# Kernel optimization log

Hardware: AMD Instinct MI355X
Metric: run time of the kernel (lower is better)

The kernel has to match this reference:

```python
import jax, jax.numpy as jnp
import numpy as np

C_M, C_Z, H, C_HID = 256, 128, 8, 32
N_SEQ, N_RES = 64, 384
INF = 1e9
EPS = 1e-5


def layernorm(x, w, b):
    mu = jnp.mean(x, axis=-1, keepdims=True)
    var = jnp.mean(jnp.square(x - mu), axis=-1, keepdims=True)
    return (x - mu) * jax.lax.rsqrt(var + EPS) * w + b


def setup_inputs() -> dict:
    key = jax.random.key(0)
    ks = jax.random.split(key, 6)
    m = jax.random.normal(ks[0], (N_SEQ, N_RES, C_M), dtype=jnp.float32)
    z = jax.random.normal(ks[1], (N_RES, N_RES, C_Z), dtype=jnp.float32)
    mask = jnp.ones((N_SEQ, N_RES), dtype=jnp.float32)
    return {
        "m": m,
        "z": z,
        "mask": mask,
        "ln_m_w": jnp.ones((C_M,), jnp.float32),
        "ln_m_b": jnp.zeros((C_M,), jnp.float32),
        "ln_z_w": jnp.ones((C_Z,), jnp.float32),
        "ln_z_b": jnp.zeros((C_Z,), jnp.float32),
        "W_z": jax.random.normal(ks[2], (C_Z, H), jnp.float32) * 0.05,
        "W_v": jax.random.normal(ks[3], (C_M, H * C_HID), jnp.float32) * 0.05,
        "W_g": jax.random.normal(ks[4], (C_M, H * C_HID), jnp.float32) * 0.05,
        "W_o": jax.random.normal(ks[5], (H * C_HID, C_M), jnp.float32) * 0.05,
    }


def reference(m, z, mask, ln_m_w, ln_m_b, ln_z_w, ln_z_b, W_z, W_v, W_g, W_o):
    S, N = m.shape[0], m.shape[1]
    # mask: max over MSA rows, keepdim -> [1, N]; bias -> [1,1,1,N]
    mask_max = jnp.max(mask, axis=-2, keepdims=True)
    mask_bias = (INF * (mask_max - 1.0))[:, None, None, :]  # [1,1,1,N]
    # pair bias: LN(z) @ W_z -> [N,N,H] -> [H,N,N]
    zb = layernorm(z, ln_z_w, ln_z_b) @ W_z  # [N,N,H]
    zb = jnp.transpose(zb, (2, 0, 1))  # [H,N,N]
    # LN on m
    m_ln = layernorm(m, ln_m_w, ln_m_b)  # [S,N,C_m]
    # values: [S,N,H*c] -> [S,H,N,c]
    v = (m_ln @ W_v).reshape(S, N, H, C_HID).transpose(0, 2, 1, 3)
    # attention weights from summed biases (no QK): [1,H,N,N] after broadcast
    a = jax.nn.softmax(mask_bias + zb[None], axis=-1)  # [1,H,N,N]
    # o = a @ v  -> [S,H,N,c]
    o = jnp.einsum('hqk,shkc->shqc', a[0], v)
    o = o.transpose(0, 2, 1, 3)  # [S,N,H,c]
    # sigmoid gate
    g = jax.nn.sigmoid(m_ln @ W_g).reshape(S, N, H, C_HID)
    o = (o * g).reshape(S, N, H * C_HID)
    return o @ W_o  # [S,N,C_m]
```

## Files before the change

### kernel.cpp

```cpp
#include <hip/hip_runtime.h>
#include <math.h>

#define S 64
#define NRES 384
#define CM 256
#define CZ 128
#define NH 8
#define CH 32
#define HC 256
#define NROW 147456

typedef unsigned short u16;
typedef __attribute__((ext_vector_type(8))) short bf16x8;
typedef __attribute__((ext_vector_type(4))) float f32x4;
typedef __attribute__((ext_vector_type(8))) unsigned short ushort8;
typedef __attribute__((ext_vector_type(4))) unsigned short ushort4_t;

#define OFF_BIAS 0
#define OFF_WWT  8192
#define OFF_C1   16384
#define OFF_C2   16448
#define OFF_WT   200704
#define OFF_WOT  462848
#define OFF_A    593920
#define OFF_VT   2953216
#define OFF_G    15536128
#define OFF_O    28119040
#define OFF_MLN  40701952
#define OFF_ZB   OFF_O

__device__ __forceinline__ u16 f2bf(float f) {
    union { float f; unsigned int u; } v; v.f = f;
    unsigned int u = v.u;
    u += 0x7fff + ((u >> 16) & 1);
    return (u16)(u >> 16);
}
__device__ __forceinline__ float bf2f(u16 b) {
    union { float f; unsigned int u; } v; v.u = ((unsigned int)b) << 16;
    return v.f;
}
__device__ __forceinline__ void gload16(const u16* g, u16* l) {
    __builtin_amdgcn_global_load_lds(
        (const __attribute__((address_space(1))) void*)g,
        (__attribute__((address_space(3))) void*)l, 16, 0, 0);
}

__global__ __launch_bounds__(256) void k_misc(
        const float* __restrict__ mask, const float* __restrict__ Wz,
        const float* __restrict__ lzw, const float* __restrict__ lzb,
        const float* __restrict__ Wv, const float* __restrict__ Wg,
        const float* __restrict__ Wo, const float* __restrict__ m,
        const float* __restrict__ lmw, const float* __restrict__ lmb,
        float* __restrict__ bias, u16* __restrict__ WWT,
        float* __restrict__ C1, float* __restrict__ C2,
        u16* __restrict__ Wt, u16* __restrict__ Wot, u16* __restrict__ mln) {
    __shared__ float sP[2][2][8];
    const int bid = blockIdx.x, tid = threadIdx.x;
    if (bid < 2) {
        const int k = bid * 256 + tid;
        if (k < NRES) {
            float mx = -1e30f;
            for (int s = 0; s < S; ++s) mx = fmaxf(mx, mask[s * NRES + k]);
            bias[k] = 1e9f * (mx - 1.0f);
        }
    } else if (bid == 2) {
        const int wave = tid >> 6, lane = tid & 63;
        if (tid < 128) {
            const int c = tid;
            const float4 wz0 = *(const float4*)&Wz[c * 8];
            const float4 wz1 = *(const float4*)&Wz[c * 8 + 4];
            const float lw = lzw[c], lbv = lzb[c];
            float wzv[8] = {wz0.x, wz0.y, wz0.z, wz0.w, wz1.x, wz1.y, wz1.z, wz1.w};
            float ww[8], wb[8];
            #pragma unroll
            for (int h = 0; h < 8; ++h) {
                ww[h] = lw * wzv[h];
                wb[h] = lbv * wzv[h];
                WWT[h * 128 + c] = f2bf(ww[h]);
                WWT[(8 + h) * 128 + c] = 0;
            }
            #pragma unroll
            for (int h = 0; h < 8; ++h) {
                #pragma unroll
                for (int off = 1; off < 64; off <<= 1) {
                    ww[h] += __shfl_xor(ww[h], off);
                    wb[h] += __shfl_xor(wb[h], off);
                }
            }
            if (lane == 0) {
                #pragma unroll
                for (int h = 0; h < 8; ++h) {
                    sP[wave][0][h] = ww[h];
                    sP[wave][1][h] = wb[h];
                }
            }
        }
        __syncthreads();
        if (tid < 8) {
            C1[tid] = sP[0][0][tid] + sP[1][0][tid];
            C2[tid] = sP[0][1][tid] + sP[1][1][tid];
        }
    } else if (bid < 515) {
        const int i = (bid - 3) * 256 + tid;
        const int n = i >> 8, k = i & 255;
        const float v = (n < HC) ? Wv[(size_t)k * HC + n] : Wg[(size_t)k * HC + (n - HC)];
        Wt[i] = f2bf(v);
    } else if (bid < 771) {
        const int i = (bid - 515) * 256 + tid;
        const int n = i >> 8, k = i & 255;
        Wot[i] = f2bf(Wo[(size_t)k * CM + n]);
    } else {
        const int row = (bid - 771) * 4 + (tid >> 6);
        const int lane = tid & 63;
        const float4 x = *(const float4*)&m[(size_t)row * CM + lane * 4];
        float sm = x.x + x.y + x.z + x.w;
        float sq = x.x*x.x + x.y*x.y + x.z*x.z + x.w*x.w;
        #pragma unroll
        for (int off = 32; off >= 1; off >>= 1) {
            sm += __shfl_xor(sm, off);
            sq += __shfl_xor(sq, off);
        }
        const float mu = sm * (1.0f / CM);
        const float var = sq * (1.0f / CM) - mu * mu;
        const float rs = rsqrtf(var + 1e-5f);
        const float4 w4 = *(const float4*)&lmw[lane * 4];
        const float4 b4 = *(const float4*)&lmb[lane * 4];
        u16 t4[4];
        t4[0] = f2bf((x.x - mu) * rs * w4.x + b4.x);
        t4[1] = f2bf((x.y - mu) * rs * w4.y + b4.y);
        t4[2] = f2bf((x.z - mu) * rs * w4.z + b4.z);
        t4[3] = f2bf((x.w - mu) * rs * w4.w + b4.w);
        *(ushort4_t*)&mln[(size_t)row * CM + lane * 4] = *(ushort4_t*)t4;
    }
}

__global__ __launch_bounds__(256) void k_zb(
        const float* __restrict__ z, const u16* __restrict__ WWT,
        const float* __restrict__ C1, const float* __restrict__ C2,
        float* __restrict__ zb) {
    __shared__ u16 sZ[4][2048];
    __shared__ float sSt[4][2][16];
    const int tid = threadIdx.x, wave = tid >> 6, lane = tid & 63;
    const int rl = lane & 15, kg = lane >> 4;
    u16* myZ = &sZ[wave][0];
    bf16x8 bfr[4];
    #pragma unroll
    for (int t = 0; t < 4; ++t)
        bfr[t] = *(const bf16x8*)&WWT[rl * 128 + t * 32 + kg * 8];
    const float c1 = (rl < 8) ? C1[rl] : 0.f;
    const float c2 = (rl < 8) ? C2[rl] : 0.f;

    #pragma unroll 1
    for (int it = 0; it < 4; ++it) {
        const int row0 = (blockIdx.x * 4 + it) * 64 + wave * 16;
        const float4* zbase = (const float4*)(z + (size_t)row0 * CZ);
        float smj[4], sqj[4];
        #pragma unroll
        for (int j = 0; j < 4; ++j) {
            const int ci = lane + 64 * j;
            const int rloc = ci >> 4, ch = ci & 15;
            const float4 x0 = zbase[ci * 2];
            const float4 x1 = zbase[ci * 2 + 1];
            float xs[8] = {x0.x, x0.y, x0.z, x0.w, x1.x, x1.y, x1.z, x1.w};
            float sm = 0.f, sq = 0.f;
            u16 t8[8];
            #pragma unroll
            for (int e = 0; e < 8; ++e) {
                sm += xs[e]; sq += xs[e] * xs[e];
                t8[e] = f2bf(xs[e]);
            }
            smj[j] = sm; sqj[j] = sq;
            *(ushort8*)&myZ[rloc * 128 + (ch ^ (rloc & 7)) * 8] = *(ushort8*)t8;
        }
        #pragma unroll
        for (int j = 0; j < 4; ++j) {
            #pragma unroll
            for (int off = 1; off < 16; off <<= 1) {
                smj[j] += __shfl_xor(smj[j], off);
                sqj[j] += __shfl_xor(sqj[j], off);
            }
        }
        if ((lane & 15) == 0) {
            #pragma unroll
            for (int j = 0; j < 4; ++j) {
                const int r = (lane >> 4) + 4 * j;
                const float mu = smj[j] * (1.0f / CZ);
                const float var = sqj[j] * (1.0f / CZ) - mu * mu;
                sSt[wave][0][r] = mu;
                sSt[wave][1][r] = rsqrtf(var + 1e-5f);
            }
        }
        bf16x8 af[4];
        #pragma unroll
        for (int t = 0; t < 4; ++t)
            af[t] = *(const bf16x8*)&myZ[rl * 128 + ((t * 4 + kg) ^ (rl & 7)) * 8];
        f32x4 acc = {};
        #pragma unroll
        for (int t = 0; t < 4; ++t)
            acc = __builtin_amdgcn_mfma_f32_16x16x32_bf16(af[t], bfr[t], acc, 0, 0, 0);
        f32x4 pv;
        #pragma unroll
        for (int r = 0; r < 4; ++r) {
            const int rr = kg * 4 + r;
            pv[r] = sSt[wave][1][rr] * (acc[r] - sSt[wave][0][rr] * c1) + c2;
        }
        if (rl < 8)
            *(f32x4*)&zb[(size_t)rl * NROW + row0 + kg * 4] = pv;
    }
}

__global__ __launch_bounds__(256) void k_stage2(
        const u16* __restrict__ mln, const u16* __restrict__ Wt,
        const float* __restrict__ zb, const float* __restrict__ bias,
        u16* __restrict__ vt, u16* __restrict__ g_, u16* __restrict__ a_out) {
    __shared__ u16 As[128][32];
    __shared__ u16 Bs[128][32];
    const int bid = blockIdx.x, tid = threadIdx.x;
    if (bid >= 768) {
        const int w = (bid - 768) * 4 + (tid >> 6);
        const int lane = tid & 63;
        const int h = w & 7, q = w >> 3;
        const float* zbh = zb + (size_t)h * NROW + (size_t)q * NRES;
        float v[6];
        float mx = -1e30f;
        #pragma unroll
        for (int t = 0; t < 6; ++t) {
            const int k = lane + 64 * t;
            v[t] = zbh[k] + bias[k];
            mx = fmaxf(mx, v[t]);
        }
        #pragma unroll
        for (int off = 32; off >= 1; off >>= 1) mx = fmaxf(mx, __shfl_xor(mx, off));
        float sum = 0.f;
        #pragma unroll
        for (int t = 0; t < 6; ++t) { v[t] = expf(v[t] - mx); sum += v[t]; }
        #pragma unroll
        for (int off = 32; off >= 1; off >>= 1) sum += __shfl_xor(sum, off);
        const float inv = 1.0f / sum;
        #pragma unroll
        for (int t = 0; t < 6; ++t)
            a_out[((size_t)h * NRES + q) * NRES + lane + 64 * t] = f2bf(v[t] * inv);
        return;
    }
    const int xcd = bid & 7, idx = bid >> 3;
    const int nt = idx & 3, mt = xcd * 24 + (idx >> 2);
    const int m0 = mt * 128, n0 = nt * 128;
    const int wave = tid >> 6, lane = tid & 63;
    const int wm = (wave >> 1) * 64, wn = (wave & 1) * 64;
    const int rl = lane & 15, kg = lane >> 4;
    const int lr = lane >> 2, lk = (lane & 3) * 8;
    const int wr = wave * 32;
    const u16* ag  = mln + (size_t)(m0 + wr + lr) * CM + lk;
    const u16* ag2 = ag + 16 * CM;
    const u16* bg  = Wt + (size_t)(n0 + wr + lr) * CM + lk;
    const u16* bg2 = bg + 16 * CM;
    u16* al  = &As[wr][0];
    u16* al2 = &As[wr + 16][0];
    u16* bl  = &Bs[wr][0];
    u16* bl2 = &Bs[wr + 16][0];
    const bool vhalf = (n0 < HC);
    f32x4 acc[4][4] = {};
    for (int kt = 0; kt < CM; kt += 32) {
        if (kt) __syncthreads();
        gload16(ag + kt, al);  gload16(ag2 + kt, al2);
        gload16(bg + kt, bl);  gload16(bg2 + kt, bl2);
        __syncthreads();
        bf16x8 af[4], bfr[4];
        #pragma unroll
        for (int i = 0; i < 4; ++i) af[i]  = *(const bf16x8*)&As[wm + i*16 + rl][kg*8];
        #pragma unroll
        for (int j = 0; j < 4; ++j) bfr[j] = *(const bf16x8*)&Bs[wn + j*16 + rl][kg*8];
        if (vhalf) {
            #pragma unroll
            for (int j = 0; j < 4; ++j)
                #pragma unroll
                for (int i = 0; i < 4; ++i)
                    acc[j][i] = __builtin_amdgcn_mfma_f32_16x16x32_bf16(bfr[j], af[i], acc[j][i], 0, 0, 0);
        } else {
            #pragma unroll
            for (int i = 0; i < 4; ++i)
                #pragma unroll
                for (int j = 0; j < 4; ++j)
                    acc[i][j] = __builtin_amdgcn_mfma_f32_16x16x32_bf16(af[i], bfr[j], acc[i][j], 0, 0, 0);
        }
    }
    if (vhalf) {
        #pragma unroll
        for (int j = 0; j < 4; ++j)
            #pragma unroll
            for (int r = 0; r < 4; ++r) {
                const int vcol = n0 + wn + j*16 + kg*4 + r;
                const int h = vcol >> 5, c = vcol & 31;
                #pragma unroll
                for (int i = 0; i < 4; ++i) {
                    const int mrowb = m0 + wm + i*16;
                    const int s = mrowb / NRES;
                    const int nn = mrowb - s * NRES + rl;
                    vt[(((size_t)h * S + s) * CH + c) * NRES + nn] = f2bf(acc[j][i][r]);
                }
            }
    } else {
        #pragma unroll
        for (int i = 0; i < 4; ++i)
            #pragma unroll
            for (int r = 0; r < 4; ++r) {
                const int row = m0 + wm + i*16 + kg*4 + r;
                #pragma unroll
                for (int j = 0; j < 4; ++j) {
                    const int gc = n0 + wn + j*16 + rl - HC;
                    g_[(size_t)row * HC + gc] = f2bf(1.0f / (1.0f + expf(-acc[i][j][r])));
                }
            }
    }
}

__global__ __launch_bounds__(256) void k_attn2(const u16* __restrict__ a_,
        const u16* __restrict__ vt, u16* __restrict__ o_) {
    __shared__ u16 As[128][32];
    __shared__ u16 Bs[128][32];
    const int tid = threadIdx.x;
    const int h = blockIdx.x & 7, rem = blockIdx.x >> 3;
    const int mt = rem >> 4, nt = rem & 15;
    const int q0 = mt * 128, sc0 = nt * 128;
    const int wave = tid >> 6, lane = tid & 63;
    const int wm = (wave >> 1) * 64, wn = (wave & 1) * 64;
    const int rl = lane & 15, kg = lane >> 4;
    const int lr = lane >> 2, lk = (lane & 3) * 8;
    const int wr = wave * 32;
    const u16* ag  = a_ + (size_t)h * NRES * NRES + (size_t)(q0 + wr + lr) * NRES + lk;
    const u16* ag2 = ag + 16 * NRES;
    const u16* bg  = vt + (size_t)h * S * CH * NRES + (size_t)(sc0 + wr + lr) * NRES + lk;
    const u16* bg2 = bg + 16 * NRES;
    u16* al  = &As[wr][0];
    u16* al2 = &As[wr + 16][0];
    u16* bl  = &Bs[wr][0];
    u16* bl2 = &Bs[wr + 16][0];
    f32x4 acc[4][4] = {};
    for (int kt = 0; kt < NRES; kt += 32) {
        if (kt) __syncthreads();
        gload16(ag + kt, al);  gload16(ag2 + kt, al2);
        gload16(bg + kt, bl);  gload16(bg2 + kt, bl2);
        __syncthreads();
        bf16x8 af[4], bfr[4];
        #pragma unroll
        for (int i = 0; i < 4; ++i) af[i]  = *(const bf16x8*)&As[wm + i*16 + rl][kg*8];
        #pragma unroll
        for (int j = 0; j < 4; ++j) bfr[j] = *(const bf16x8*)&Bs[wn + j*16 + rl][kg*8];
        #pragma unroll
        for (int i = 0; i < 4; ++i)
            #pragma unroll
            for (int j = 0; j < 4; ++j)
                acc[i][j] = __builtin_amdgcn_mfma_f32_16x16x32_bf16(af[i], bfr[j], acc[i][j], 0, 0, 0);
    }
    #pragma unroll
    for (int i = 0; i < 4; ++i)
        #pragma unroll
        for (int r = 0; r < 4; ++r) {
            const int q = q0 + wm + i*16 + kg*4 + r;
            #pragma unroll
            for (int j = 0; j < 4; ++j) {
                const int sc = sc0 + wn + j*16 + rl;
                const int s = sc >> 5, c = sc & 31;
                o_[(((size_t)s * NRES + q) * NH + h) * CH + c] = f2bf(acc[i][j][r]);
            }
        }
}

__global__ __launch_bounds__(256) void k_gemm_out(const u16* __restrict__ o_,
        const u16* __restrict__ g_, const u16* __restrict__ Wot,
        float* __restrict__ out) {
    __shared__ u16 As[128][40];
    __shared__ u16 Bs[128][32];
    const int tid = threadIdx.x;
    const int xcd = blockIdx.x & 7, idx = blockIdx.x >> 3;
    const int nt = idx & 1, mt = xcd * 24 + (idx >> 1);
    const int m0 = mt * 128, n0 = nt * 128;
    const int wave = tid >> 6, lane = tid & 63;
    const int wm = (wave >> 1) * 64, wn = (wave & 1) * 64;
    const int rl = lane & 15, kg = lane >> 4;
    const int lr = lane >> 2, lk = (lane & 3) * 8;
    const int wr = wave * 32;
    const int sr = tid >> 1, sh = (tid & 1) * 16;
    const u16* orow = o_ + (size_t)(m0 + sr) * HC;
    const u16* grow = g_ + (size_t)(m0 + sr) * HC;
    const u16* bg  = Wot + (size_t)(n0 + wr + lr) * HC + lk;
    const u16* bg2 = bg + 16 * HC;
    u16* bl  = &Bs[wr][0];
    u16* bl2 = &Bs[wr + 16][0];
    f32x4 acc[4][4] = {};
    for (int kt = 0; kt < HC; kt += 32) {
        if (kt) __syncthreads();
        gload16(bg + kt, bl);  gload16(bg2 + kt, bl2);
        {
            u16 tmp[16];
            const ushort8 ov0 = *(const ushort8*)&orow[kt + sh];
            const ushort8 ov1 = *(const ushort8*)&orow[kt + sh + 8];
            const ushort8 gv0 = *(const ushort8*)&grow[kt + sh];
            const ushort8 gv1 = *(const ushort8*)&grow[kt + sh + 8];
            #pragma unroll
            for (int p = 0; p < 8; ++p) {
                tmp[p]     = f2bf(bf2f(ov0[p]) * bf2f(gv0[p]));
                tmp[p + 8] = f2bf(bf2f(ov1[p]) * bf2f(gv1[p]));
            }
            *(ushort8*)&As[sr][sh]     = *(ushort8*)&tmp[0];
            *(ushort8*)&As[sr][sh + 8] = *(ushort8*)&tmp[8];
        }
        __syncthreads();
        bf16x8 af[4], bfr[4];
        #pragma unroll
        for (int i = 0; i < 4; ++i) af[i]  = *(const bf16x8*)&As[wm + i*16 + rl][kg*8];
        #pragma unroll
        for (int j = 0; j < 4; ++j) bfr[j] = *(const bf16x8*)&Bs[wn + j*16 + rl][kg*8];
        #pragma unroll
        for (int i = 0; i < 4; ++i)
            #pragma unroll
            for (int j = 0; j < 4; ++j)
                acc[i][j] = __builtin_amdgcn_mfma_f32_16x16x32_bf16(af[i], bfr[j], acc[i][j], 0, 0, 0);
    }
    #pragma unroll
    for (int i = 0; i < 4; ++i)
        #pragma unroll
        for (int r = 0; r < 4; ++r) {
            const int row = m0 + wm + i*16 + kg*4 + r;
            #pragma unroll
            for (int j = 0; j < 4; ++j)
                out[(size_t)row * CM + n0 + wn + j*16 + rl] = acc[i][j][r];
        }
}

extern "C" void kernel_launch(void* const* d_in, const int* in_sizes, int n_in,
                              void* d_out, int out_size, void* d_ws, size_t ws_size,
                              hipStream_t stream) {
    const float* m      = (const float*)d_in[0];
    const float* z      = (const float*)d_in[1];
    const float* mask   = (const float*)d_in[2];
    const float* ln_m_w = (const float*)d_in[3];
    const float* ln_m_b = (const float*)d_in[4];
    const float* ln_z_w = (const float*)d_in[5];
    const float* ln_z_b = (const float*)d_in[6];
    const float* Wz     = (const float*)d_in[7];
    const float* Wv     = (const float*)d_in[8];
    const float* Wg     = (const float*)d_in[9];
    const float* Wo     = (const float*)d_in[10];
    float* out = (float*)d_out;
    char* ws = (char*)d_ws;

    float* bias = (float*)(ws + OFF_BIAS);
    u16* WWT    = (u16*)(ws + OFF_WWT);
    float* C1   = (float*)(ws + OFF_C1);
    float* C2   = (float*)(ws + OFF_C2);
    u16* Wt     = (u16*)(ws + OFF_WT);
    u16* Wot    = (u16*)(ws + OFF_WOT);
    u16* a      = (u16*)(ws + OFF_A);
    u16* vtw    = (u16*)(ws + OFF_VT);
    u16* gw     = (u16*)(ws + OFF_G);
    u16* ow     = (u16*)(ws + OFF_O);
    u16* mlnw   = (u16*)(ws + OFF_MLN);
    float* zbw  = (float*)(ws + OFF_ZB);

    k_misc<<<6915, 256, 0, stream>>>(mask, Wz, ln_z_w, ln_z_b, Wv, Wg, Wo, m,
                                     ln_m_w, ln_m_b, bias, WWT, C1, C2, Wt, Wot, mlnw);
    k_zb<<<576, 256, 0, stream>>>(z, WWT, C1, C2, zbw);
    k_stage2<<<1536, 256, 0, stream>>>(mlnw, Wt, zbw, bias, vtw, gw, a);
    k_attn2<<<384, 256, 0, stream>>>(a, vtw, ow);
    k_gemm_out<<<384, 256, 0, stream>>>(ow, gw, Wot, out);
}
```

Measured before the change: 85.45 us.

## Spread z-bias kernel over more blocks with up-front loads, parallelize mask max

The pair-bias kernel drops its 4-iteration loop per block and launches four times as many blocks, each handling one 64-row tile. Each thread issues all eight float4 loads of its tile up front, so more memory traffic is in flight at once. The per-row statistics now reduce across 32 lanes with contiguous float4 loads instead of strided 8-wide chunks. The mask max-reduction is split across 6 blocks and 4 waves, with a shared-memory combine replacing the serial 64-row loop per thread.

New measurement: 76.59 us. 10.4% less time.

```diff
diff --git a/kernel.cpp b/kernel.cpp
--- a/kernel.cpp
+++ b/kernel.cpp
@@ -45,7 +45,7 @@
         (__attribute__((address_space(3))) void*)l, 16, 0, 0);
 }
 
-__global__ __launch_bounds__(256) void k_misc(
+__global__ __launch_bounds__(256) void k_pre(
         const float* __restrict__ mask, const float* __restrict__ Wz,
         const float* __restrict__ lzw, const float* __restrict__ lzb,
         const float* __restrict__ Wv, const float* __restrict__ Wg,
@@ -54,17 +54,26 @@
         float* __restrict__ bias, u16* __restrict__ WWT,
         float* __restrict__ C1, float* __restrict__ C2,
         u16* __restrict__ Wt, u16* __restrict__ Wot, u16* __restrict__ mln) {
-    __shared__ float sP[2][2][8];
+    __shared__ float sRed[4][64];
     const int bid = blockIdx.x, tid = threadIdx.x;
-    if (bid < 2) {
-        const int k = bid * 256 + tid;
-        if (k < NRES) {
-            float mx = -1e30f;
-            for (int s = 0; s < S; ++s) mx = fmaxf(mx, mask[s * NRES + k]);
+    const int wave = tid >> 6, lane = tid & 63;
+    if (bid < 6) {
+        const int k = bid * 64 + lane;
+        float mx = -1e30f;
+        #pragma unroll
+        for (int i = 0; i < 16; ++i) {
+            const int s = wave * 16 + i;
+            mx = fmaxf(mx, mask[(size_t)s * NRES + k]);
+        }
+        sRed[wave][lane] = mx;
+        __syncthreads();
+        if (wave == 0) {
+            mx = fmaxf(fmaxf(sRed[0][lane], sRed[1][lane]),
+                       fmaxf(sRed[2][lane], sRed[3][lane]));
             bias[k] = 1e9f * (mx - 1.0f);
         }
-    } else if (bid == 2) {
-        const int wave = tid >> 6, lane = tid & 63;
+    } else if (bid == 6) {
+        __shared__ float sP[2][2][8];
         if (tid < 128) {
             const int c = tid;
             const float4 wz0 = *(const float4*)&Wz[c * 8];
@@ -100,18 +109,17 @@
             C1[tid] = sP[0][0][tid] + sP[1][0][tid];
             C2[tid] = sP[0][1][tid] + sP[1][1][tid];
         }
-    } else if (bid < 515) {
-        const int i = (bid - 3) * 256 + tid;
+    } else if (bid < 519) {
+        const int i = (bid - 7) * 256 + tid;
         const int n = i >> 8, k = i & 255;
         const float v = (n < HC) ? Wv[(size_t)k * HC + n] : Wg[(size_t)k * HC + (n - HC)];
         Wt[i] = f2bf(v);
-    } else if (bid < 771) {
-        const int i = (bid - 515) * 256 + tid;
+    } else if (bid < 775) {
+        const int i = (bid - 519) * 256 + tid;
         const int n = i >> 8, k = i & 255;
         Wot[i] = f2bf(Wo[(size_t)k * CM + n]);
     } else {
-        const int row = (bid - 771) * 4 + (tid >> 6);
-        const int lane = tid & 63;
+        const int row = (bid - 775) * 4 + wave;
         const float4 x = *(const float4*)&m[(size_t)row * CM + lane * 4];
         float sm = x.x + x.y + x.z + x.w;
         float sq = x.x*x.x + x.y*x.y + x.z*x.z + x.w*x.w;
@@ -143,70 +151,69 @@
     const int tid = threadIdx.x, wave = tid >> 6, lane = tid & 63;
     const int rl = lane & 15, kg = lane >> 4;
     u16* myZ = &sZ[wave][0];
+    const int row0 = blockIdx.x * 64 + wave * 16;
+    const float4* zbase = (const float4*)(z + (size_t)row0 * CZ);
+    float4 xb[8];
+    #pragma unroll
+    for (int j = 0; j < 8; ++j) xb[j] = zbase[lane + 64 * j];
     bf16x8 bfr[4];
     #pragma unroll
     for (int t = 0; t < 4; ++t)
         bfr[t] = *(const bf16x8*)&WWT[rl * 128 + t * 32 + kg * 8];
     const float c1 = (rl < 8) ? C1[rl] : 0.f;
     const float c2 = (rl < 8) ? C2[rl] : 0.f;
-
-    #pragma unroll 1
-    for (int it = 0; it < 4; ++it) {
-        const int row0 = (blockIdx.x * 4 + it) * 64 + wave * 16;
-        const float4* zbase = (const float4*)(z + (size_t)row0 * CZ);
-        float smj[4], sqj[4];
-        #pragma unroll
-        for (int j = 0; j < 4; ++j) {
-            const int ci = lane + 64 * j;
-            const int rloc = ci >> 4, ch = ci & 15;
-            const float4 x0 = zbase[ci * 2];
-            const float4 x1 = zbase[ci * 2 + 1];
-            float xs[8] = {x0.x, x0.y, x0.z, x0.w, x1.x, x1.y, x1.z, x1.w};
-            float sm = 0.f, sq = 0.f;
-            u16 t8[8];
-            #pragma unroll
-            for (int e = 0; e < 8; ++e) {
-                sm += xs[e]; sq += xs[e] * xs[e];
-                t8[e] = f2bf(xs[e]);
-            }
-            smj[j] = sm; sqj[j] = sq;
-            *(ushort8*)&myZ[rloc * 128 + (ch ^ (rloc & 7)) * 8] = *(ushort8*)t8;
-        }
-        #pragma unroll
-        for (int j = 0; j < 4; ++j) {
-            #pragma unroll
-            for (int off = 1; off < 16; off <<= 1) {
-                smj[j] += __shfl_xor(smj[j], off);
-                sqj[j] += __shfl_xor(sqj[j], off);
-            }
-        }
-        if ((lane & 15) == 0) {
-            #pragma unroll
-            for (int j = 0; j < 4; ++j) {
-                const int r = (lane >> 4) + 4 * j;
-                const float mu = smj[j] * (1.0f / CZ);
-                const float var = sqj[j] * (1.0f / CZ) - mu * mu;
-                sSt[wave][0][r] = mu;
-                sSt[wave][1][r] = rsqrtf(var + 1e-5f);
-            }
-        }
-        bf16x8 af[4];
-        #pragma unroll
-        for (int t = 0; t < 4; ++t)
-            af[t] = *(const bf16x8*)&myZ[rl * 128 + ((t * 4 + kg) ^ (rl & 7)) * 8];
-        f32x4 acc = {};
-        #pragma unroll
-        for (int t = 0; t < 4; ++t)
-            acc = __builtin_amdgcn_mfma_f32_16x16x32_bf16(af[t], bfr[t], acc, 0, 0, 0);
-        f32x4 pv;
-        #pragma unroll
-        for (int r = 0; r < 4; ++r) {
-            const int rr = kg * 4 + r;
-            pv[r] = sSt[wave][1][rr] * (acc[r] - sSt[wave][0][rr] * c1) + c2;
-        }
-        if (rl < 8)
-            *(f32x4*)&zb[(size_t)rl * NROW + row0 + kg * 4] = pv;
-    }
+    const int hw = lane >> 5, c4 = lane & 31;
+    float smj[8], sqj[8];
+    #pragma unroll
+    for (int j = 0; j < 8; ++j) {
+        const int r = 2 * j + hw;
+        const float4 x = xb[j];
+        float xs[4] = {x.x, x.y, x.z, x.w};
+        float sm = 0.f, sq = 0.f;
+        u16 t4[4];
+        #pragma unroll
+        for (int e = 0; e < 4; ++e) {
+            sm += xs[e]; sq += xs[e] * xs[e];
+            t4[e] = f2bf(xs[e]);
+        }
+        smj[j] = sm; sqj[j] = sq;
+        *(ushort4_t*)&myZ[r * 128 + ((c4 >> 1) ^ (r & 7)) * 8 + (c4 & 1) * 4] =
+            *(ushort4_t*)t4;
+    }
+    #pragma unroll
+    for (int j = 0; j < 8; ++j) {
+        #pragma unroll
+        for (int off = 1; off < 32; off <<= 1) {
+            smj[j] += __shfl_xor(smj[j], off);
+            sqj[j] += __shfl_xor(sqj[j], off);
+        }
+    }
+    if ((lane & 31) == 0) {
+        #pragma unroll
+        for (int j = 0; j < 8; ++j) {
+            const int r = 2 * j + hw;
+            const float mu = smj[j] * (1.0f / CZ);
+            const float var = sqj[j] * (1.0f / CZ) - mu * mu;
+            sSt[wave][0][r] = mu;
+            sSt[wave][1][r] = rsqrtf(var + 1e-5f);
+        }
+    }
+    bf16x8 af[4];
+    #pragma unroll
+    for (int t = 0; t < 4; ++t)
+        af[t] = *(const bf16x8*)&myZ[rl * 128 + ((t * 4 + kg) ^ (rl & 7)) * 8];
+    f32x4 acc = {};
+    #pragma unroll
+    for (int t = 0; t < 4; ++t)
+        acc = __builtin_amdgcn_mfma_f32_16x16x32_bf16(af[t], bfr[t], acc, 0, 0, 0);
+    f32x4 pv;
+    #pragma unroll
+    for (int r = 0; r < 4; ++r) {
+        const int rr = kg * 4 + r;
+        pv[r] = sSt[wave][1][rr] * (acc[r] - sSt[wave][0][rr] * c1) + c2;
+    }
+    if (rl < 8)
+        *(f32x4*)&zb[(size_t)rl * NROW + row0 + kg * 4] = pv;
 }
 
 __global__ __launch_bounds__(256) void k_stage2(
@@ -458,9 +465,9 @@
     u16* mlnw   = (u16*)(ws + OFF_MLN);
     float* zbw  = (float*)(ws + OFF_ZB);
 
-    k_misc<<<6915, 256, 0, stream>>>(mask, Wz, ln_z_w, ln_z_b, Wv, Wg, Wo, m,
-                                     ln_m_w, ln_m_b, bias, WWT, C1, C2, Wt, Wot, mlnw);
-    k_zb<<<576, 256, 0, stream>>>(z, WWT, C1, C2, zbw);
+    k_pre<<<6919, 256, 0, stream>>>(mask, Wz, ln_z_w, ln_z_b, Wv, Wg, Wo, m,
+                                    ln_m_w, ln_m_b, bias, WWT, C1, C2, Wt, Wot, mlnw);
+    k_zb<<<2304, 256, 0, stream>>>(z, WWT, C1, C2, zbw);
     k_stage2<<<1536, 256, 0, stream>>>(mlnw, Wt, zbw, bias, vtw, gw, a);
     k_attn2<<<384, 256, 0, stream>>>(a, vtw, ow);
     k_gemm_out<<<384, 256, 0, stream>>>(ow, gw, Wot, out);
```
